# Optimization experiments

Hardware: AMD Instinct MI355X
Metric: run time of the kernel (lower is better)

The kernel has to match this reference:

```python
import jax, jax.numpy as jnp
import numpy as np

TEMPERATURE = 0.5
NORMALIZE = True


def setup_inputs() -> dict:
    key = jax.random.key(0)
    k1, k2 = jax.random.split(key)
    bs, d = 4096, 256
    zi = jax.random.normal(k1, (bs, d), dtype=jnp.float32)
    zj = jax.random.normal(k2, (bs, d), dtype=jnp.float32)
    return {"zi": zi, "zj": zj}


def _off_diag(m):
    # gather off-diagonal entries of [bs, bs] matrix into [bs, bs-1]
    bs = m.shape[0]
    rows = jnp.arange(bs)[:, None]
    cols = jnp.arange(bs - 1)[None, :]
    idx = cols + (cols >= rows)  # skip the diagonal column per row
    return jnp.take_along_axis(m, idx, axis=1)


def reference(zi, zj):
    bs = zi.shape[0]
    if NORMALIZE:
        zi = zi / jnp.linalg.norm(zi, axis=-1, keepdims=True)
        zj = zj / jnp.linalg.norm(zj, axis=-1, keepdims=True)
    inv_t = 1.0 / TEMPERATURE
    logits_ii = (zi @ zi.T) * inv_t
    logits_ij = (zi @ zj.T) * inv_t
    logits_ji = (zj @ zi.T) * inv_t
    logits_jj = (zj @ zj.T) * inv_t

    pos = jnp.concatenate([jnp.diag(logits_ij), jnp.diag(logits_ji)], axis=0)[:, None]  # [2bs,1]
    neg_i = jnp.concatenate([_off_diag(logits_ii), _off_diag(logits_ij)], axis=1)  # [bs, 2(bs-1)]
    neg_j = jnp.concatenate([_off_diag(logits_ji), _off_diag(logits_jj)], axis=1)
    neg = jnp.concatenate([neg_i, neg_j], axis=0)  # [2bs, 2(bs-1)]
    logits = jnp.concatenate([pos, neg], axis=1)  # [2bs, 2bs-1]

    # cross-entropy with all labels == 0 (the positive is column 0)
    loss = jnp.mean(jax.nn.logsumexp(logits, axis=1) - logits[:, 0])
    return loss
```

## Files before the change

kernel.cpp:

```cpp
#include <hip/hip_runtime.h>
#include <hip/hip_bf16.h>

#define BS 4096
#define D 256
#define NROW 8192
#define INV_T 2.0f

typedef short short8 __attribute__((ext_vector_type(8)));
typedef float f32x4 __attribute__((ext_vector_type(4)));

__device__ __forceinline__ unsigned short f2b(float x) {
    __hip_bfloat16 h = __float2bfloat16(x);
    return *reinterpret_cast<unsigned short*>(&h);
}
__device__ __forceinline__ float b2f(unsigned short b) {
    unsigned int u = ((unsigned int)b) << 16;
    return __uint_as_float(u);
}

__global__ __launch_bounds__(256) void k_norm(const float* __restrict__ zi,
                                              const float* __restrict__ zj,
                                              unsigned short* __restrict__ W,
                                              float* __restrict__ rowsum,
                                              float* __restrict__ accum) {
    const int gt   = blockIdx.x * 256 + threadIdx.x;
    const int wave = gt >> 6;
    const int lane = threadIdx.x & 63;

    const float* src = (wave < BS) ? (zi + (size_t)wave * D)
                                   : (zj + (size_t)(wave - BS) * D);
    float4 v = reinterpret_cast<const float4*>(src)[lane];
    float ss = v.x * v.x + v.y * v.y + v.z * v.z + v.w * v.w;
#pragma unroll
    for (int m = 1; m < 64; m <<= 1) ss += __shfl_xor(ss, m, 64);
    float inv = rsqrtf(ss);

    ushort4 o;
    o.x = f2b(v.x * inv);
    o.y = f2b(v.y * inv);
    o.z = f2b(v.z * inv);
    o.w = f2b(v.w * inv);
    reinterpret_cast<ushort4*>(W + (size_t)wave * D)[lane] = o;

    if (gt < NROW) rowsum[gt] = 0.0f;
    if (gt < 2)    accum[gt]  = 0.0f;
}

__global__ __launch_bounds__(256, 4) void k_gemm(const unsigned short* __restrict__ W,
                                                 float* __restrict__ rowsum) {
    __shared__ unsigned short lA[128 * 64];
    __shared__ unsigned short lB[128 * 64];

    const int tid  = threadIdx.x;
    const int lane = tid & 63;
    const int w    = tid >> 6;
    const int wr   = w >> 1;
    const int wc   = w & 1;

    const int t = blockIdx.x;
    const int u = 2079 - t;
    int ri = (int)((sqrtf(8.0f * (float)u + 1.0f) - 1.0f) * 0.5f);
    while ((ri + 1) * (ri + 2) / 2 <= u) ++ri;
    while (ri * (ri + 1) / 2 > u) --ri;
    const int bi = 63 - ri;
    const int bj = 63 - (u - ri * (ri + 1) / 2);
    const int rowBase = bi * 128;
    const int colBase = bj * 128;
    const bool isDiag = (bi == bj);

    f32x4 acc[4][4] = {};

    const int srcColElems = (((lane & 7) ^ ((lane >> 3) & 7)) * 8);
    const int rowInSeg = (lane >> 3);

    for (int kk = 0; kk < 4; ++kk) {
        const int kBase = kk * 64;
        __syncthreads();
#pragma unroll
        for (int c = 0; c < 4; ++c) {
            const int seg = c * 4 + w;
            const int row = seg * 8 + rowInSeg;
            const unsigned short* gA = W + (size_t)(rowBase + row) * D + kBase + srcColElems;
            const unsigned short* gB = W + (size_t)(colBase + row) * D + kBase + srcColElems;
            __builtin_amdgcn_global_load_lds(
                (const __attribute__((address_space(1))) void*)gA,
                (__attribute__((address_space(3))) void*)(lA + seg * 512), 16, 0, 0);
            __builtin_amdgcn_global_load_lds(
                (const __attribute__((address_space(1))) void*)gB,
                (__attribute__((address_space(3))) void*)(lB + seg * 512), 16, 0, 0);
        }
        __syncthreads();

#pragma unroll
        for (int ks = 0; ks < 2; ++ks) {
            short8 a[4], b[4];
            const int swz = lane & 7;
            const int logChunk = ks * 4 + (lane >> 4);
#pragma unroll
            for (int mi = 0; mi < 4; ++mi) {
                const int r = wr * 64 + mi * 16 + (lane & 15);
                a[mi] = *reinterpret_cast<const short8*>(lA + r * 64 + ((logChunk ^ swz) * 8));
            }
#pragma unroll
            for (int ni = 0; ni < 4; ++ni) {
                const int r = wc * 64 + ni * 16 + (lane & 15);
                b[ni] = *reinterpret_cast<const short8*>(lB + r * 64 + ((logChunk ^ swz) * 8));
            }
#pragma unroll
            for (int mi = 0; mi < 4; ++mi)
#pragma unroll
                for (int ni = 0; ni < 4; ++ni)
                    acc[mi][ni] = __builtin_amdgcn_mfma_f32_16x16x32_bf16(
                        a[mi], b[ni], acc[mi][ni], 0, 0, 0);
        }
    }

    float colacc[4] = {0.f, 0.f, 0.f, 0.f};
#pragma unroll
    for (int mi = 0; mi < 4; ++mi) {
#pragma unroll
        for (int j = 0; j < 4; ++j) {
            const int gr = rowBase + wr * 64 + mi * 16 + (lane >> 4) * 4 + j;
            float s = 0.0f;
#pragma unroll
            for (int ni = 0; ni < 4; ++ni) {
                float e;
                if (isDiag) {
                    const int gc = colBase + wc * 64 + ni * 16 + (lane & 15);
                    e = (gr == gc) ? 0.0f : __expf(acc[mi][ni][j] * INV_T);
                } else {
                    e = __expf(acc[mi][ni][j] * INV_T);
                }
                s += e;
                colacc[ni] += e;
            }
            s += __shfl_xor(s, 1, 64);
            s += __shfl_xor(s, 2, 64);
            s += __shfl_xor(s, 4, 64);
            s += __shfl_xor(s, 8, 64);
            if ((lane & 15) == 0) atomicAdd(&rowsum[gr], s);
        }
    }
    if (!isDiag) {
#pragma unroll
        for (int ni = 0; ni < 4; ++ni) {
            float cs = colacc[ni];
            cs += __shfl_xor(cs, 16, 64);
            cs += __shfl_xor(cs, 32, 64);
            if ((lane >> 4) == 0)
                atomicAdd(&rowsum[colBase + wc * 64 + ni * 16 + lane], cs);
        }
    }
}

__global__ __launch_bounds__(256) void k_finalize(const unsigned short* __restrict__ W,
                                                  const float* __restrict__ rowsum,
                                                  float* __restrict__ accum) {
    const int tid  = blockIdx.x * 256 + threadIdx.x;
    const int lane = threadIdx.x & 63;

    float l = logf(rowsum[tid]);
#pragma unroll
    for (int m = 1; m < 64; m <<= 1) l += __shfl_xor(l, m, 64);
    if (lane == 0) atomicAdd(&accum[0], l);

    const int wgid = tid >> 6;
    float pacc = 0.0f;
    for (int t = 0; t < 32; ++t) {
        const int i = wgid * 32 + t;
        ushort4 ub = reinterpret_cast<const ushort4*>(W + (size_t)i * D)[lane];
        ushort4 vb = reinterpret_cast<const ushort4*>(W + (size_t)(BS + i) * D)[lane];
        pacc += b2f(ub.x) * b2f(vb.x) + b2f(ub.y) * b2f(vb.y)
              + b2f(ub.z) * b2f(vb.z) + b2f(ub.w) * b2f(vb.w);
    }
#pragma unroll
    for (int m = 1; m < 64; m <<= 1) pacc += __shfl_xor(pacc, m, 64);
    if (lane == 0) atomicAdd(&accum[1], INV_T * pacc);
}

__global__ void k_write(const float* __restrict__ accum, float* __restrict__ out) {
    out[0] = accum[0] * (1.0f / NROW) - accum[1] * (1.0f / BS);
}

extern "C" void kernel_launch(void* const* d_in, const int* in_sizes, int n_in,
                              void* d_out, int out_size, void* d_ws, size_t ws_size,
                              hipStream_t stream) {
    const float* zi = (const float*)d_in[0];
    const float* zj = (const float*)d_in[1];
    float* out = (float*)d_out;

    unsigned short* W = (unsigned short*)d_ws;
    float* rowsum = (float*)((char*)d_ws + (size_t)NROW * D * 2);
    float* accum  = rowsum + NROW;

    k_norm<<<NROW / 4, 256, 0, stream>>>(zi, zj, W, rowsum, accum);
    k_gemm<<<2080, 256, 0, stream>>>(W, rowsum);
    k_finalize<<<32, 256, 0, stream>>>(W, rowsum, accum);
    k_write<<<1, 1, 0, stream>>>(accum, out);
}
```

Measured before the change: 107.0 us.

## Double-buffer GEMM LDS loads and fold final write into finalize kernel

The GEMM kernel now uses two LDS buffers and prefetches the next two K-slices with global_load_lds, waiting on vmcnt before each compute step. This overlaps global-to-LDS transfers with MFMA work instead of serializing load, barrier and compute. LDS per block doubles and launch bounds drop to 2 blocks per CU, which reduces occupancy. Separately, the tiny k_write launch is removed: the last finalize block, found through an atomic counter, writes the output.

```diff
diff --git a/kernel.cpp b/kernel.cpp
--- a/kernel.cpp
+++ b/kernel.cpp
@@ -43,13 +43,12 @@
     reinterpret_cast<ushort4*>(W + (size_t)wave * D)[lane] = o;
 
     if (gt < NROW) rowsum[gt] = 0.0f;
-    if (gt < 2)    accum[gt]  = 0.0f;
-}
-
-__global__ __launch_bounds__(256, 4) void k_gemm(const unsigned short* __restrict__ W,
+    if (gt < 3)    accum[gt]  = 0.0f;
+}
+
+__global__ __launch_bounds__(256, 2) void k_gemm(const unsigned short* __restrict__ W,
                                                  float* __restrict__ rowsum) {
-    __shared__ unsigned short lA[128 * 64];
-    __shared__ unsigned short lB[128 * 64];
+    __shared__ unsigned short lds[2][2][128 * 64];
 
     const int tid  = threadIdx.x;
     const int lane = tid & 63;
@@ -73,24 +72,35 @@
     const int srcColElems = (((lane & 7) ^ ((lane >> 3) & 7)) * 8);
     const int rowInSeg = (lane >> 3);
 
+#define STAGE(p, kk) do {                                                          \
+    const int kBase_ = (kk) * 64;                                                  \
+    _Pragma("unroll")                                                              \
+    for (int c = 0; c < 4; ++c) {                                                  \
+        const int seg = c * 4 + w;                                                 \
+        const int row = seg * 8 + rowInSeg;                                        \
+        const unsigned short* gA = W + (size_t)(rowBase + row) * D + kBase_ + srcColElems; \
+        const unsigned short* gB = W + (size_t)(colBase + row) * D + kBase_ + srcColElems; \
+        __builtin_amdgcn_global_load_lds(                                          \
+            (const __attribute__((address_space(1))) void*)gA,                     \
+            (__attribute__((address_space(3))) void*)(&lds[p][0][seg * 512]), 16, 0, 0); \
+        __builtin_amdgcn_global_load_lds(                                          \
+            (const __attribute__((address_space(1))) void*)gB,                     \
+            (__attribute__((address_space(3))) void*)(&lds[p][1][seg * 512]), 16, 0, 0); \
+    }                                                                              \
+} while (0)
+
+    STAGE(0, 0);
+    STAGE(1, 1);
+
     for (int kk = 0; kk < 4; ++kk) {
-        const int kBase = kk * 64;
-        __syncthreads();
-#pragma unroll
-        for (int c = 0; c < 4; ++c) {
-            const int seg = c * 4 + w;
-            const int row = seg * 8 + rowInSeg;
-            const unsigned short* gA = W + (size_t)(rowBase + row) * D + kBase + srcColElems;
-            const unsigned short* gB = W + (size_t)(colBase + row) * D + kBase + srcColElems;
-            __builtin_amdgcn_global_load_lds(
-                (const __attribute__((address_space(1))) void*)gA,
-                (__attribute__((address_space(3))) void*)(lA + seg * 512), 16, 0, 0);
-            __builtin_amdgcn_global_load_lds(
-                (const __attribute__((address_space(1))) void*)gB,
-                (__attribute__((address_space(3))) void*)(lB + seg * 512), 16, 0, 0);
-        }
-        __syncthreads();
-
+        const int p = kk & 1;
+        if (kk < 3) { asm volatile("s_waitcnt vmcnt(8)" ::: "memory"); }
+        else        { asm volatile("s_waitcnt vmcnt(0)" ::: "memory"); }
+        __builtin_amdgcn_s_barrier();
+        __builtin_amdgcn_sched_barrier(0);
+
+        const unsigned short* pA = &lds[p][0][0];
+        const unsigned short* pB = &lds[p][1][0];
 #pragma unroll
         for (int ks = 0; ks < 2; ++ks) {
             short8 a[4], b[4];
@@ -99,12 +109,12 @@
 #pragma unroll
             for (int mi = 0; mi < 4; ++mi) {
                 const int r = wr * 64 + mi * 16 + (lane & 15);
-                a[mi] = *reinterpret_cast<const short8*>(lA + r * 64 + ((logChunk ^ swz) * 8));
+                a[mi] = *reinterpret_cast<const short8*>(pA + r * 64 + ((logChunk ^ swz) * 8));
             }
 #pragma unroll
             for (int ni = 0; ni < 4; ++ni) {
                 const int r = wc * 64 + ni * 16 + (lane & 15);
-                b[ni] = *reinterpret_cast<const short8*>(lB + r * 64 + ((logChunk ^ swz) * 8));
+                b[ni] = *reinterpret_cast<const short8*>(pB + r * 64 + ((logChunk ^ swz) * 8));
             }
 #pragma unroll
             for (int mi = 0; mi < 4; ++mi)
@@ -113,7 +123,11 @@
                     acc[mi][ni] = __builtin_amdgcn_mfma_f32_16x16x32_bf16(
                         a[mi], b[ni], acc[mi][ni], 0, 0, 0);
         }
-    }
+
+        __builtin_amdgcn_s_barrier();
+        if (kk < 2) STAGE(p, kk + 2);
+    }
+#undef STAGE
 
     float colacc[4] = {0.f, 0.f, 0.f, 0.f};
 #pragma unroll
@@ -155,7 +169,8 @@
 
 __global__ __launch_bounds__(256) void k_finalize(const unsigned short* __restrict__ W,
                                                   const float* __restrict__ rowsum,
-                                                  float* __restrict__ accum) {
+                                                  float* __restrict__ accum,
+                                                  float* __restrict__ out) {
     const int tid  = blockIdx.x * 256 + threadIdx.x;
     const int lane = threadIdx.x & 63;
 
@@ -176,10 +191,17 @@
 #pragma unroll
     for (int m = 1; m < 64; m <<= 1) pacc += __shfl_xor(pacc, m, 64);
     if (lane == 0) atomicAdd(&accum[1], INV_T * pacc);
-}
-
-__global__ void k_write(const float* __restrict__ accum, float* __restrict__ out) {
-    out[0] = accum[0] * (1.0f / NROW) - accum[1] * (1.0f / BS);
+
+    __syncthreads();
+    if (threadIdx.x == 0) {
+        __threadfence();
+        int* done = (int*)(accum + 2);
+        if (atomicAdd(done, 1) == 31) {
+            float a0 = atomicAdd(&accum[0], 0.0f);
+            float a1 = atomicAdd(&accum[1], 0.0f);
+            out[0] = a0 * (1.0f / NROW) - a1 * (1.0f / BS);
+        }
+    }
 }
 
 extern "C" void kernel_launch(void* const* d_in, const int* in_sizes, int n_in,
@@ -195,6 +217,5 @@
 
     k_norm<<<NROW / 4, 256, 0, stream>>>(zi, zj, W, rowsum, accum);
     k_gemm<<<2080, 256, 0, stream>>>(W, rowsum);
-    k_finalize<<<32, 256, 0, stream>>>(W, rowsum, accum);
-    k_write<<<1, 1, 0, stream>>>(accum, out);
-}
+    k_finalize<<<32, 256, 0, stream>>>(W, rowsum, accum, out);
+}
```

After: 118.5 us. 10.7% more time.
